# Optimization experiments

Measured on AMD Instinct MI355X. Metric: run time of the kernel, lower is better.

## Reference

```python
import jax, jax.numpy as jnp
import numpy as np

D = 128; H = 4; C = 128; L = 4
NC = 65536   # cells (1024 graphs x 64 cells)
NP = 32768   # pieces
NE = 65536   # edges per cell->cell direction
B = 1024     # num graphs
BW = 7       # BOARD_WIDTH (undefined global in source; connect-four width)
SLOPE = 0.2  # GATv2 LeakyReLU negative slope


def setup_inputs() -> dict:
    key = jax.random.key(0)
    ks = jax.random.split(key, 24)
    s = 0.05
    return {
        'cell_x': jnp.zeros((NC,), dtype=jnp.int32),
        'piece_x': jax.random.randint(ks[0], (NP,), 0, 2, dtype=jnp.int32),
        'occ_src': jax.random.randint(ks[1], (NP,), 0, NP, dtype=jnp.int32),
        'occ_dst': jax.random.randint(ks[2], (NP,), 0, NC, dtype=jnp.int32),
        'en_src': jax.random.randint(ks[3], (NE,), 0, NC, dtype=jnp.int32),
        'en_dst': jax.random.randint(ks[4], (NE,), 0, NC, dtype=jnp.int32),
        'ee_src': jax.random.randint(ks[5], (NE,), 0, NC, dtype=jnp.int32),
        'ee_dst': jax.random.randint(ks[6], (NE,), 0, NC, dtype=jnp.int32),
        'cell_batch': (jnp.arange(NC, dtype=jnp.int32) // (NC // B)).astype(jnp.int32),
        'cell_emb': jax.random.normal(ks[7], (1, D), jnp.float32),
        'piece_emb': jax.random.normal(ks[8], (2, D), jnp.float32),
        'Wl': jax.random.normal(ks[9], (L, 3, D, H * C), jnp.float32) * s,
        'bl': jnp.zeros((L, 3, H * C), jnp.float32),
        'Wr': jax.random.normal(ks[10], (L, 3, D, H * C), jnp.float32) * s,
        'br': jnp.zeros((L, 3, H * C), jnp.float32),
        'att': jax.random.normal(ks[11], (L, 3, H, C), jnp.float32) * 0.1,
        'conv_bias': jnp.zeros((L, 3, C), jnp.float32),
        'fc1_W': jax.random.normal(ks[12], (D, 64), jnp.float32) * s,
        'fc1_b': jnp.zeros((64,), jnp.float32),
        'pol_W': jax.random.normal(ks[13], (64, BW), jnp.float32) * s,
        'pol_b': jnp.zeros((BW,), jnp.float32),
        'val_W': jax.random.normal(ks[14], (64, 1), jnp.float32) * s,
        'val_b': jnp.zeros((1,), jnp.float32),
    }


def _gatv2(x_src, x_dst, src, dst, Wl, bl, Wr, br, att, bias):
    # PyG GATv2Conv, concat=False (mean over heads), add_self_loops=False, eval-mode dropout.
    n_dst = x_dst.shape[0]
    xl = (x_src @ Wl + bl).reshape(-1, H, C)      # [Ns,H,C]
    xr = (x_dst @ Wr + br).reshape(n_dst, H, C)   # [Nd,H,C]
    e = jax.nn.leaky_relu(xl[src] + xr[dst], SLOPE)            # [E,H,C]
    score = jnp.einsum('ehc,hc->eh', e, att)                   # [E,H]
    m = jax.ops.segment_max(score, dst, num_segments=n_dst)    # [Nd,H]
    p = jnp.exp(score - m[dst])
    denom = jax.ops.segment_sum(p, dst, num_segments=n_dst)
    alpha = p / (denom[dst] + 1e-16)                           # scatter-softmax
    out = jax.ops.segment_sum(alpha[:, :, None] * xl[src], dst, num_segments=n_dst)  # [Nd,H,C]
    return out.mean(axis=1) + bias


def reference(cell_x, piece_x, occ_src, occ_dst, en_src, en_dst, ee_src, ee_dst,
              cell_batch, cell_emb, piece_emb, Wl, bl, Wr, br, att, conv_bias,
              fc1_W, fc1_b, pol_W, pol_b, val_W, val_b):
    cell = cell_emb[cell_x]    # [NC,D]
    piece = piece_emb[piece_x]  # [NP,D]
    rels = [(occ_src, occ_dst), (en_src, en_dst), (ee_src, ee_dst)]
    for l in range(L):
        acc = jnp.zeros_like(cell)
        for r, (src, dst) in enumerate(rels):
            x_src = piece if r == 0 else cell
            acc = acc + _gatv2(x_src, cell, src, dst, Wl[l, r], bl[l, r],
                               Wr[l, r], br[l, r], att[l, r], conv_bias[l, r])
        cell = jax.nn.relu(acc)  # HeteroConv aggr='sum', then relu; dropout is identity in eval
    # global mean pool over cells per graph
    sums = jax.ops.segment_sum(cell, cell_batch, num_segments=B)
    cnts = jax.ops.segment_sum(jnp.ones((cell.shape[0],), cell.dtype), cell_batch, num_segments=B)
    pooled = sums / jnp.maximum(cnts, 1.0)[:, None]            # [B,D]
    h = jax.nn.relu(pooled @ fc1_W + fc1_b)
    policy_logits = h @ pol_W + pol_b
    value = jnp.tanh(h @ val_W + val_b)
    return policy_logits, value
```

## Files before the change

kernel.cpp:

```cpp
#include <hip/hip_runtime.h>
#include <hip/hip_bf16.h>
#include <math.h>

#define NCELLS 65536
#define NPIECE 32768
#define NEDGE  65536
#define NGRAPH 1024
#define DIM    128
#define NH     4
#define CH     128
#define HC     512
#define NLAYER 4
#define SLOPE  0.2f
#define DCAP   16

#define SCAP0   16384
#define SCAP12  36864
#define HCAP0   8192
#define HCAP12  20480
#define YCAP0   20480
#define YCAP12  28672
#define XLC_OFF0 0
#define XLC_OFF1 16384
#define XLC_OFF2 53248
#define XRC_OFF0 0
#define XRC_OFF1 8192
#define XRC_OFF2 28672
#define YL_OFF0  0
#define YL_OFF1  20480
#define YL_OFF2  49152
#define GEMM_BLOCKS 4960

typedef __attribute__((ext_vector_type(8))) __bf16 bf16x8;
typedef __attribute__((ext_vector_type(4))) float f32x4;

__device__ inline float bf2f(unsigned int u) {
    return __uint_as_float(u << 16);
}
__device__ inline unsigned short f2bf(float f) {
    unsigned int x = __float_as_uint(f);
    unsigned int r = (x + 0x7fff + ((x >> 16) & 1)) >> 16;
    return (unsigned short)r;
}
__device__ __forceinline__ void unpack8(uint4 v, float* o) {
    o[0] = bf2f(v.x & 0xffff); o[1] = bf2f(v.x >> 16);
    o[2] = bf2f(v.y & 0xffff); o[3] = bf2f(v.y >> 16);
    o[4] = bf2f(v.z & 0xffff); o[5] = bf2f(v.z >> 16);
    o[6] = bf2f(v.w & 0xffff); o[7] = bf2f(v.w >> 16);
}

#define GLOBAL_AS __attribute__((address_space(1)))
#define LDS_AS __attribute__((address_space(3)))
__device__ __forceinline__ void async_cp16(const void* g, void* l) {
    __builtin_amdgcn_global_load_lds((const GLOBAL_AS unsigned int*)g,
                                     (LDS_AS unsigned int*)l, 16, 0, 0);
}

__global__ void fill_kernel(float* __restrict__ p, float v, long n) {
    long i = (long)blockIdx.x * 256 + threadIdx.x;
    if (i < n) p[i] = v;
}

__global__ void embed_bf16_kernel(const int* __restrict__ idx, const float* __restrict__ emb,
                                  unsigned short* __restrict__ outb) {
    long t = (long)blockIdx.x * 256 + threadIdx.x;
    int node = (int)(t >> 7);
    int c = (int)(t & 127);
    outb[t] = f2bf(emb[(size_t)idx[node] * DIM + c]);
}

__global__ __launch_bounds__(256) void wconv_kernel(const float* __restrict__ Wl,
                                                    const float* __restrict__ Wr,
                                                    unsigned short* __restrict__ Wt) {
    __shared__ float tile[16][17];
    int bid = blockIdx.x;
    int wi = bid >> 8;
    int rem = bid & 255;
    int kt = rem >> 5;
    int nt = rem & 31;
    int tx = threadIdx.x & 15, ty = threadIdx.x >> 4;
    const float* W = (wi < 12) ? (Wl + (size_t)wi * DIM * HC) : (Wr + (size_t)(wi - 12) * DIM * HC);
    tile[ty][tx] = W[(size_t)(kt * 16 + ty) * HC + nt * 16 + tx];
    __syncthreads();
    Wt[(size_t)wi * HC * DIM + (size_t)(nt * 16 + ty) * DIM + kt * 16 + tx] = f2bf(tile[tx][ty]);
}

__global__ __launch_bounds__(256) void wsum_kernel(const float* __restrict__ Wl,
                                                   const float* __restrict__ bl,
                                                   unsigned short* __restrict__ Wsumt,
                                                   float* __restrict__ bsum) {
    int wi = blockIdx.x;
    const float* W = Wl + (size_t)wi * DIM * HC;
    for (int base = 0; base < 16384; base += 256) {
        int idx = base + threadIdx.x;
        int c = idx & 127, k = idx >> 7;
        float s = 0.25f * (W[(size_t)k * HC + c] + W[(size_t)k * HC + 128 + c] +
                           W[(size_t)k * HC + 256 + c] + W[(size_t)k * HC + 384 + c]);
        Wsumt[(size_t)wi * 16384 + (size_t)c * 128 + k] = f2bf(s);
    }
    if (threadIdx.x < 128) {
        int c = threadIdx.x;
        const float* b = bl + (size_t)wi * HC;
        bsum[wi * 128 + c] = 0.25f * (b[c] + b[128 + c] + b[256 + c] + b[384 + c]);
    }
}

__global__ __launch_bounds__(256) void bucket_build(const int* __restrict__ occ_src,
                                                    const int* __restrict__ occ_dst,
                                                    const int* __restrict__ en_src,
                                                    const int* __restrict__ en_dst,
                                                    const int* __restrict__ ee_src,
                                                    const int* __restrict__ ee_dst,
                                                    int* __restrict__ cnt3,
                                                    int* __restrict__ bucket3) {
    int id = blockIdx.x * 256 + threadIdx.x;
    int rel, e;
    const int* dstp;
    const int* srcp;
    if (id < NPIECE) { rel = 0; e = id; dstp = occ_dst; srcp = occ_src; }
    else if (id < NPIECE + NEDGE) { rel = 1; e = id - NPIECE; dstp = en_dst; srcp = en_src; }
    else if (id < NPIECE + 2 * NEDGE) { rel = 2; e = id - NPIECE - NEDGE; dstp = ee_dst; srcp = ee_src; }
    else return;
    int d = dstp[e];
    int pos = atomicAdd(&cnt3[rel * NCELLS + d], 1);
    if (pos < DCAP) bucket3[(size_t)rel * NCELLS * DCAP + (size_t)d * DCAP + pos] = srcp[e];
}

__global__ __launch_bounds__(256) void mark_build(const int* __restrict__ occ_src,
                                                  const int* __restrict__ occ_dst,
                                                  const int* __restrict__ en_src,
                                                  const int* __restrict__ en_dst,
                                                  const int* __restrict__ ee_src,
                                                  const int* __restrict__ ee_dst,
                                                  const int* __restrict__ cnt3,
                                                  int* __restrict__ srcmark,
                                                  int* __restrict__ ymark) {
    int id = blockIdx.x * 256 + threadIdx.x;
    int rel, e;
    const int* dstp;
    const int* srcp;
    if (id < NPIECE) { rel = 0; e = id; dstp = occ_dst; srcp = occ_src; }
    else if (id < NPIECE + NEDGE) { rel = 1; e = id - NPIECE; dstp = en_dst; srcp = en_src; }
    else if (id < NPIECE + 2 * NEDGE) { rel = 2; e = id - NPIECE - NEDGE; dstp = ee_dst; srcp = ee_src; }
    else return;
    int c = cnt3[rel * NCELLS + dstp[e]];
    if (c >= 2) srcmark[(rel << 16) + srcp[e]] = 1;
    else ymark[(rel << 16) + srcp[e]] = 1;
}

__global__ __launch_bounds__(256) void compact_all(const int* __restrict__ cnt3,
                                                   const int* __restrict__ srcmark,
                                                   const int* __restrict__ ymark,
                                                   unsigned long long* __restrict__ pcounts,
                                                   int* __restrict__ hotlist,
                                                   int* __restrict__ hotpos,
                                                   int* __restrict__ srclist,
                                                   int* __restrict__ srcpos,
                                                   int* __restrict__ ylist,
                                                   int* __restrict__ ypos) {
    __shared__ int wcnt[4][3];
    __shared__ unsigned long long blockbase;
    int id = blockIdx.x * 256 + threadIdx.x;
    int lane = threadIdx.x & 63;
    int w = threadIdx.x >> 6;
    int r = id >> 16;
    int node = id & (NCELLS - 1);

    bool a0 = (cnt3[id] >= 2);
    bool a1 = (srcmark[id] != 0);
    bool a2 = (ymark[id] != 0);
    unsigned long long m0 = __ballot(a0);
    unsigned long long m1 = __ballot(a1);
    unsigned long long m2 = __ballot(a2);
    if (lane == 0) {
        wcnt[w][0] = (int)__popcll(m0);
        wcnt[w][1] = (int)__popcll(m1);
        wcnt[w][2] = (int)__popcll(m2);
    }
    __syncthreads();
    if (threadIdx.x == 0) {
        unsigned long long s0 = wcnt[0][0] + wcnt[1][0] + wcnt[2][0] + wcnt[3][0];
        unsigned long long s1 = wcnt[0][1] + wcnt[1][1] + wcnt[2][1] + wcnt[3][1];
        unsigned long long s2 = wcnt[0][2] + wcnt[1][2] + wcnt[2][2] + wcnt[3][2];
        blockbase = atomicAdd(&pcounts[r], s0 | (s1 << 21) | (s2 << 42));
    }
    __syncthreads();
    unsigned long long bb = blockbase;
    int b0 = (int)(bb & 0x1FFFFF);
    int b1 = (int)((bb >> 21) & 0x1FFFFF);
    int b2 = (int)((bb >> 42) & 0x1FFFFF);
#pragma unroll
    for (int w2 = 0; w2 < 4; w2++) {
        if (w2 < w) { b0 += wcnt[w2][0]; b1 += wcnt[w2][1]; b2 += wcnt[w2][2]; }
    }
    {
        int cap  = (r == 0) ? HCAP0 : HCAP12;
        int loff = (r == 0) ? XRC_OFF0 : (r == 1) ? XRC_OFF1 : XRC_OFF2;
        if (a0) {
            int pos = b0 + (int)__popcll(m0 & ((1ull << lane) - 1ull));
            if (pos < cap) { hotlist[loff + pos] = node; hotpos[id] = pos; }
            else hotpos[id] = cap - 1;
        }
    }
    {
        int cap  = (r == 0) ? SCAP0 : SCAP12;
        int loff = (r == 0) ? XLC_OFF0 : (r == 1) ? XLC_OFF1 : XLC_OFF2;
        if (a1) {
            int pos = b1 + (int)__popcll(m1 & ((1ull << lane) - 1ull));
            if (pos < cap) { srclist[loff + pos] = node; srcpos[id] = pos; }
            else srcpos[id] = cap - 1;
        }
    }
    {
        int cap  = (r == 0) ? YCAP0 : YCAP12;
        int loff = (r == 0) ? YL_OFF0 : (r == 1) ? YL_OFF1 : YL_OFF2;
        if (a2) {
            int pos = b2 + (int)__popcll(m2 & ((1ull << lane) - 1ull));
            if (pos < cap) { ylist[loff + pos] = node; ypos[id] = pos; }
            else ypos[id] = cap - 1;
        }
    }
}

__global__ void unpack_counts(const unsigned long long* __restrict__ pcounts,
                              int* __restrict__ counts) {
    int r = threadIdx.x;
    if (r < 3) {
        unsigned long long v = pcounts[r];
        counts[r]     = (int)(v & 0x1FFFFF);
        counts[4 + r] = (int)((v >> 21) & 0x1FFFFF);
        counts[8 + r] = (int)((v >> 42) & 0x1FFFFF);
    }
}

__global__ __launch_bounds__(256) void bucket_translate(const int* __restrict__ cnt3,
                                                        const int* __restrict__ srcpos,
                                                        const int* __restrict__ ypos,
                                                        int* __restrict__ bucket3) {
    int id = blockIdx.x * 256 + threadIdx.x;
    if (id >= 3 * NCELLS) return;
    int r = id >> 16;
    int deg = cnt3[id];
    if (deg > DCAP) deg = DCAP;
    if (deg == 0) return;
    int* b = bucket3 + (size_t)id * DCAP;
    if (deg == 1) {
        b[0] = ypos[(r << 16) + b[0]];
    } else {
        for (int s = 0; s < deg; s++) b[s] = srcpos[(r << 16) + b[s]];
    }
}

__device__ __forceinline__ void gemm_body(const unsigned short* __restrict__ A,
                                          const int* __restrict__ gather, int nrows,
                                          const unsigned short* __restrict__ Bt,
                                          const float* __restrict__ bias,
                                          unsigned short* __restrict__ out, int ostride,
                                          int row0, int col0,
                                          unsigned short* smem) {
    unsigned short* As = smem;
    unsigned short* Bs = smem + 16384;
    const int t = threadIdx.x;
    const int w = t >> 6;
    const int l = t & 63;
    const int q = l >> 4, r15 = l & 15;

    {
#pragma unroll
        for (int it = 0; it < 8; it++) {
            int r0 = 32 * w + 4 * it;
            int row = r0 + q;
            int c = r15 ^ (row & 15);
            int grow = row0 + row;
            if (gather) grow = gather[grow < nrows ? grow : (nrows - 1)];
            async_cp16(A + (size_t)grow * 128 + c * 8, &As[r0 * 128]);
        }
        const unsigned short* Bg = Bt + (size_t)col0 * 128;
#pragma unroll
        for (int it = 0; it < 4; it++) {
            int r0 = 16 * w + 4 * it;
            int row = r0 + q;
            int c = r15 ^ (row & 15);
            async_cp16(Bg + (size_t)row * 128 + c * 8, &Bs[r0 * 128]);
        }
    }
    __syncthreads();

    const int m0 = (w >> 1) * 64;
    const int n0 = (w & 1) * 32;

    f32x4 acc[2][4][2];
#pragma unroll
    for (int nh = 0; nh < 2; nh++)
#pragma unroll
        for (int i = 0; i < 4; i++)
#pragma unroll
            for (int j = 0; j < 2; j++) acc[nh][i][j] = (f32x4)(0.0f);

#pragma unroll
    for (int ks = 0; ks < 4; ks++) {
        int slot = (4 * ks + q) ^ r15;
        bf16x8 a[4], b[2];
#pragma unroll
        for (int i = 0; i < 4; i++)
            a[i] = *(const bf16x8*)&As[(m0 + 16 * i + r15) * 128 + slot * 8];
#pragma unroll
        for (int j = 0; j < 2; j++)
            b[j] = *(const bf16x8*)&Bs[(n0 + 16 * j + r15) * 128 + slot * 8];
#pragma unroll
        for (int i = 0; i < 4; i++)
#pragma unroll
            for (int j = 0; j < 2; j++)
                acc[0][i][j] = __builtin_amdgcn_mfma_f32_16x16x32_bf16(a[i], b[j], acc[0][i][j], 0, 0, 0);
    }
    __syncthreads();

    {
        const unsigned short* Bg = Bt + (size_t)(col0 + 64) * 128;
#pragma unroll
        for (int it = 0; it < 4; it++) {
            int r0 = 16 * w + 4 * it;
            int row = r0 + q;
            int c = r15 ^ (row & 15);
            async_cp16(Bg + (size_t)row * 128 + c * 8, &Bs[r0 * 128]);
        }
    }
    __syncthreads();

#pragma unroll
    for (int ks = 0; ks < 4; ks++) {
        int slot = (4 * ks + q) ^ r15;
        bf16x8 a[4], b[2];
#pragma unroll
        for (int i = 0; i < 4; i++)
            a[i] = *(const bf16x8*)&As[(m0 + 16 * i + r15) * 128 + slot * 8];
#pragma unroll
        for (int j = 0; j < 2; j++)
            b[j] = *(const bf16x8*)&Bs[(n0 + 16 * j + r15) * 128 + slot * 8];
#pragma unroll
        for (int i = 0; i < 4; i++)
#pragma unroll
            for (int j = 0; j < 2; j++)
                acc[1][i][j] = __builtin_amdgcn_mfma_f32_16x16x32_bf16(a[i], b[j], acc[1][i][j], 0, 0, 0);
    }
    __syncthreads();

    unsigned short* tile = smem;
#pragma unroll
    for (int nh = 0; nh < 2; nh++)
#pragma unroll
        for (int j = 0; j < 2; j++) {
            int col = nh * 64 + n0 + 16 * j + r15;
            float bv = bias[col0 + col];
#pragma unroll
            for (int i = 0; i < 4; i++) {
                int mg = m0 + 16 * i + 4 * q;
#pragma unroll
                for (int rg = 0; rg < 4; rg++)
                    tile[(mg + rg) * 136 + col] = f2bf(acc[nh][i][j][rg] + bv);
            }
        }
    __syncthreads();
#pragma unroll
    for (int it = 0; it < 8; it++) {
        int rr = it * 16 + (t >> 4);
        int cc = (t & 15) * 8;
        if (row0 + rr < nrows) {
            uint4 v = *(const uint4*)&tile[rr * 136 + cc];
            *(uint4*)&out[(size_t)(row0 + rr) * ostride + col0 + cc] = v;
        }
    }
}

__global__ __launch_bounds__(256) void gemm_layer(const unsigned short* __restrict__ pieceb,
                                                  const unsigned short* __restrict__ cellb,
                                                  const int* __restrict__ srclist,
                                                  const int* __restrict__ hotlist,
                                                  const int* __restrict__ ylist,
                                                  const int* __restrict__ counts,
                                                  const unsigned short* __restrict__ Wt,
                                                  const unsigned short* __restrict__ Wsumt,
                                                  const float* __restrict__ bl,
                                                  const float* __restrict__ br,
                                                  const float* __restrict__ bsum,
                                                  unsigned short* __restrict__ xlc,
                                                  unsigned short* __restrict__ yl,
                                                  unsigned short* __restrict__ xrc,
                                                  int lay) {
    __shared__ unsigned short smem[24576];
    int x = blockIdx.x;
    int r, sec, idx;
    if (x < 928) {
        r = 0;
        if (x < 512) { sec = 0; idx = x; }
        else if (x < 672) { sec = 1; idx = x - 512; }
        else { sec = 2; idx = x - 672; }
    } else if (x < 2944) {
        r = 1; x -= 928;
        if (x < 1152) { sec = 0; idx = x; }
        else if (x < 1376) { sec = 1; idx = x - 1152; }
        else { sec = 2; idx = x - 1376; }
    } else {
        r = 2; x -= 2944;
        if (x < 1152) { sec = 0; idx = x; }
        else if (x < 1376) { sec = 1; idx = x - 1152; }
        else { sec = 2; idx = x - 1376; }
    }
    int wi = lay * 3 + r;
    const unsigned short* Asrc = (r == 0) ? pieceb : cellb;
    int scap = (r == 0) ? SCAP0 : SCAP12;
    int hcap = (r == 0) ? HCAP0 : HCAP12;
    int ycap = (r == 0) ? YCAP0 : YCAP12;
    int xlcoff = (r == 0) ? XLC_OFF0 : (r == 1) ? XLC_OFF1 : XLC_OFF2;
    int xrcoff = (r == 0) ? XRC_OFF0 : (r == 1) ? XRC_OFF1 : XRC_OFF2;
    int yloff  = (r == 0) ? YL_OFF0  : (r == 1) ? YL_OFF1  : YL_OFF2;

    if (sec == 0) {
        int nrowblk = scap >> 7;
        int row = idx % nrowblk, col = idx / nrowblk;
        int nsrc = counts[4 + r];
        if (nsrc > scap) nsrc = scap;
        if (row * 128 >= nsrc) return;
        gemm_body(Asrc, srclist + xlcoff, nsrc,
                  Wt + (size_t)wi * HC * DIM, bl + (size_t)wi * HC,
                  xlc + (size_t)xlcoff * HC, HC, row * 128, col * 128, smem);
    } else if (sec == 1) {
        int ny = counts[8 + r];
        if (ny > ycap) ny = ycap;
        if (idx * 128 >= ny) return;
        gemm_body(Asrc, ylist + yloff, ny,
                  Wsumt + (size_t)wi * 16384, bsum + (size_t)wi * 128,
                  yl + (size_t)yloff * 128, 128, idx * 128, 0, smem);
    } else {
        int nrowblk = hcap >> 7;
        int row = idx % nrowblk, col = idx / nrowblk;
        int nhot = counts[r];
        if (nhot > hcap) nhot = hcap;
        if (row * 128 >= nhot) return;
        gemm_body(cellb, hotlist + xrcoff, nhot,
                  Wt + (size_t)(12 + wi) * HC * DIM, br + (size_t)wi * HC,
                  xrc + (size_t)xrcoff * HC, HC, row * 128, col * 128, smem);
    }
}

__global__ __launch_bounds__(256) void agg3(const unsigned short* __restrict__ xlc,
                                            const unsigned short* __restrict__ yl,
                                            const unsigned short* __restrict__ xrc,
                                            const int* __restrict__ bucket3,
                                            const int* __restrict__ cnt3,
                                            const int* __restrict__ hotpos,
                                            const float* __restrict__ att,
                                            const float* __restrict__ cb,
                                            unsigned short* __restrict__ cellb,
                                            int lay) {
    int d = blockIdx.x * 4 + (threadIdx.x >> 6);
    int l = threadIdx.x & 63;
    int g = l >> 4;

    int deg[3], spv[3], hp[3];
#pragma unroll
    for (int r = 0; r < 3; r++) {
        int c = cnt3[r * NCELLS + d];
        deg[r] = (c > DCAP) ? DCAP : c;
    }
#pragma unroll
    for (int r = 0; r < 3; r++)
        spv[r] = (l < deg[r]) ? bucket3[(size_t)r * NCELLS * DCAP + (size_t)d * DCAP + l] : 0;
#pragma unroll
    for (int r = 0; r < 3; r++)
        hp[r] = (deg[r] >= 2) ? hotpos[r * NCELLS + d] : 0;

    float acc[8] = {0.f, 0.f, 0.f, 0.f, 0.f, 0.f, 0.f, 0.f};
#pragma unroll
    for (int r = 0; r < 3; r++) {
        if (deg[r] == 0) continue;
        int xlcoff = (r == 0) ? XLC_OFF0 : (r == 1) ? XLC_OFF1 : XLC_OFF2;
        int xrcoff = (r == 0) ? XRC_OFF0 : (r == 1) ? XRC_OFF1 : XRC_OFF2;
        int yloff  = (r == 0) ? YL_OFF0  : (r == 1) ? YL_OFF1  : YL_OFF2;

        if (deg[r] == 1) {
            int yp = __shfl(spv[r], 0, 64);
            if (g == r) {
                uint4 v = *(const uint4*)(yl + (size_t)(yloff + yp) * 128 + (l & 15) * 8);
                float y[8];
                unpack8(v, y);
#pragma unroll
                for (int j = 0; j < 8; j++) acc[j] += y[j];
            }
        } else {
            uint4 rv = *(const uint4*)(xrc + (size_t)(xrcoff + hp[r]) * HC + l * 8);
            float re[8];
            unpack8(rv, re);
            const float* at = att + (size_t)(lay * 3 + r) * HC;
            float4 a0 = *(const float4*)&at[l * 8];
            float4 a1 = *(const float4*)&at[l * 8 + 4];
            float av[8] = {a0.x, a0.y, a0.z, a0.w, a1.x, a1.y, a1.z, a1.w};

            int dg = deg[r];
            float sum_w = 0.f;
            float tm[8] = {0.f, 0.f, 0.f, 0.f, 0.f, 0.f, 0.f, 0.f};
            int sp0 = __shfl(spv[r], 0, 64);
            uint4 vcur = *(const uint4*)(xlc + (size_t)(xlcoff + sp0) * HC + l * 8);
            for (int k = 0; k < dg; k++) {
                uint4 vnext;
                if (k + 1 < dg) {
                    int spn = __shfl(spv[r], k + 1, 64);
                    vnext = *(const uint4*)(xlc + (size_t)(xlcoff + spn) * HC + l * 8);
                }
                float le[8];
                unpack8(vcur, le);
                float partial = 0.f;
#pragma unroll
                for (int j = 0; j < 8; j++) {
                    float e = le[j] + re[j];
                    e = e > 0.0f ? e : SLOPE * e;
                    partial += e * av[j];
                }
#pragma unroll
                for (int off = 1; off < 16; off <<= 1) partial += __shfl_xor(partial, off, 64);
                float wgt = __expf(partial);
                sum_w += wgt;
#pragma unroll
                for (int j = 0; j < 8; j++) tm[j] += wgt * le[j];
                vcur = vnext;
            }
            float inv = 0.25f / sum_w;
#pragma unroll
            for (int j = 0; j < 8; j++) acc[j] += tm[j] * inv;
        }
    }

#pragma unroll
    for (int j = 0; j < 8; j++) {
        acc[j] += __shfl_xor(acc[j], 16, 64);
        acc[j] += __shfl_xor(acc[j], 32, 64);
    }

    if (l < 16) {
        int c0 = l * 8;
        float v[8];
#pragma unroll
        for (int j = 0; j < 8; j++) {
            int c = c0 + j;
            float b = cb[c] + cb[CH + c] + cb[2 * CH + c];
            v[j] = fmaxf(acc[j] + b, 0.0f);
        }
        uint4 pv;
        pv.x = (unsigned)f2bf(v[0]) | ((unsigned)f2bf(v[1]) << 16);
        pv.y = (unsigned)f2bf(v[2]) | ((unsigned)f2bf(v[3]) << 16);
        pv.z = (unsigned)f2bf(v[4]) | ((unsigned)f2bf(v[5]) << 16);
        pv.w = (unsigned)f2bf(v[6]) | ((unsigned)f2bf(v[7]) << 16);
        *(uint4*)&cellb[(size_t)d * CH + c0] = pv;
    }
}

__global__ __launch_bounds__(64) void pool_kernel(const unsigned short* __restrict__ cellb,
                                                  float* __restrict__ pooled) {
    int b = blockIdx.x, l = threadIdx.x;
    const unsigned short* base = cellb + (size_t)b * 64 * DIM;
    float s[8] = {0.f, 0.f, 0.f, 0.f, 0.f, 0.f, 0.f, 0.f};
    for (int i = 0; i < 64; i++) {
        uint4 v = *(const uint4*)(base + (size_t)i * DIM + (l & 15) * 8);
        float y[8];
        unpack8(v, y);
#pragma unroll
        for (int j = 0; j < 8; j++) s[j] += y[j];
    }
    if (l < 16) {
        float4 o0 = make_float4(s[0] * (1.f / 64.f), s[1] * (1.f / 64.f),
                                s[2] * (1.f / 64.f), s[3] * (1.f / 64.f));
        float4 o1 = make_float4(s[4] * (1.f / 64.f), s[5] * (1.f / 64.f),
                                s[6] * (1.f / 64.f), s[7] * (1.f / 64.f));
        *(float4*)&pooled[(size_t)b * DIM + l * 8] = o0;
        *(float4*)&pooled[(size_t)b * DIM + l * 8 + 4] = o1;
    }
}

__global__ __launch_bounds__(64) void head_kernel(const float* __restrict__ pooled,
                                                  const float* __restrict__ fc1W,
                                                  const float* __restrict__ fc1b,
                                                  const float* __restrict__ polW,
                                                  const float* __restrict__ polb,
                                                  const float* __restrict__ valW,
                                                  const float* __restrict__ valb,
                                                  float* __restrict__ out) {
    int b = blockIdx.x, t = threadIdx.x;
    __shared__ float ps[128];
    __shared__ float hs[64];
    ps[t] = pooled[(size_t)b * DIM + t];
    ps[t + 64] = pooled[(size_t)b * DIM + 64 + t];
    __syncthreads();
    float h = fc1b[t];
#pragma unroll 16
    for (int d = 0; d < 128; d++) h += ps[d] * fc1W[d * 64 + t];
    hs[t] = fmaxf(h, 0.0f);
    __syncthreads();
    if (t < 7) {
        float po = polb[t];
#pragma unroll 16
        for (int k = 0; k < 64; k++) po += hs[k] * polW[k * 7 + t];
        out[(size_t)b * 7 + t] = po;
    }
    if (t == 63) {
        float v = valb[0];
#pragma unroll 16
        for (int k = 0; k < 64; k++) v += hs[k] * valW[k];
        out[(size_t)NGRAPH * 7 + b] = tanhf(v);
    }
}

extern "C" void kernel_launch(void* const* d_in, const int* in_sizes, int n_in,
                              void* d_out, int out_size, void* d_ws, size_t ws_size,
                              hipStream_t stream) {
    const int* cell_x   = (const int*)d_in[0];
    const int* piece_x  = (const int*)d_in[1];
    const int* occ_src  = (const int*)d_in[2];
    const int* occ_dst  = (const int*)d_in[3];
    const int* en_src   = (const int*)d_in[4];
    const int* en_dst   = (const int*)d_in[5];
    const int* ee_src   = (const int*)d_in[6];
    const int* ee_dst   = (const int*)d_in[7];
    const float* cell_emb  = (const float*)d_in[9];
    const float* piece_emb = (const float*)d_in[10];
    const float* Wl  = (const float*)d_in[11];
    const float* bl  = (const float*)d_in[12];
    const float* Wr  = (const float*)d_in[13];
    const float* br  = (const float*)d_in[14];
    const float* att = (const float*)d_in[15];
    const float* conv_bias = (const float*)d_in[16];
    const float* fc1W = (const float*)d_in[17];
    const float* fc1b = (const float*)d_in[18];
    const float* polW = (const float*)d_in[19];
    const float* polb = (const float*)d_in[20];
    const float* valW = (const float*)d_in[21];
    const float* valb = (const float*)d_in[22];
    float* out = (float*)d_out;

    char* ws = (char*)d_ws;
    size_t off = 0;
    auto take = [&](size_t bytes) -> void* {
        void* p = (void*)(ws + off);
        off += (bytes + 255) & ~(size_t)255;
        return p;
    };
    unsigned short* cellb  = (unsigned short*)take((size_t)NCELLS * DIM * 2);
    unsigned short* pieceb = (unsigned short*)take((size_t)NPIECE * DIM * 2);
    unsigned short* xlc    = (unsigned short*)take((size_t)(SCAP0 + 2 * SCAP12) * HC * 2);
    unsigned short* yl     = (unsigned short*)take((size_t)(YCAP0 + 2 * YCAP12) * 128 * 2);
    unsigned short* xrc    = (unsigned short*)take((size_t)(HCAP0 + 2 * HCAP12) * HC * 2);
    unsigned short* Wt     = (unsigned short*)take((size_t)24 * HC * DIM * 2);
    unsigned short* Wsumt  = (unsigned short*)take((size_t)12 * 128 * 128 * 2);
    float* bsum            = (float*)take((size_t)12 * 128 * 4);
    int*   izone   = (int*)take(((size_t)9 * NCELLS + 32) * 4);
    int*   cnt3    = izone;
    unsigned long long* pcounts = (unsigned long long*)(izone + 3 * NCELLS);
    int*   counts  = izone + 3 * NCELLS + 8;
    int*   srcmark = izone + 3 * NCELLS + 32;
    int*   ymark   = izone + 6 * NCELLS + 32;
    int*   bucket3 = (int*)take((size_t)3 * NCELLS * DCAP * 4);
    int*   hotlist = (int*)take((size_t)(HCAP0 + 2 * HCAP12) * 4);
    int*   hotpos  = (int*)take((size_t)3 * NCELLS * 4);
    int*   srclist = (int*)take((size_t)(SCAP0 + 2 * SCAP12) * 4);
    int*   srcpos  = (int*)take((size_t)3 * NCELLS * 4);
    int*   ylist   = (int*)take((size_t)(YCAP0 + 2 * YCAP12) * 4);
    int*   ypos    = (int*)take((size_t)3 * NCELLS * 4);
    float* pooled  = (float*)take((size_t)NGRAPH * DIM * 4);

    if (off > ws_size) {
        fill_kernel<<<(out_size + 255) / 256, 256, 0, stream>>>(out, 0.0f, out_size);
        return;
    }

    wconv_kernel<<<24 * 256, 256, 0, stream>>>(Wl, Wr, Wt);
    wsum_kernel<<<12, 256, 0, stream>>>(Wl, bl, Wsumt, bsum);
    embed_bf16_kernel<<<NPIECE * DIM / 256, 256, 0, stream>>>(piece_x, piece_emb, pieceb);
    embed_bf16_kernel<<<NCELLS * DIM / 256, 256, 0, stream>>>(cell_x, cell_emb, cellb);
    fill_kernel<<<(9 * NCELLS + 32 + 255) / 256, 256, 0, stream>>>((float*)izone, 0.0f, 9 * NCELLS + 32);
    bucket_build<<<(NPIECE + 2 * NEDGE + 255) / 256, 256, 0, stream>>>(
        occ_src, occ_dst, en_src, en_dst, ee_src, ee_dst, cnt3, bucket3);
    mark_build<<<(NPIECE + 2 * NEDGE + 255) / 256, 256, 0, stream>>>(
        occ_src, occ_dst, en_src, en_dst, ee_src, ee_dst, cnt3, srcmark, ymark);
    compact_all<<<3 * NCELLS / 256, 256, 0, stream>>>(
        cnt3, srcmark, ymark, pcounts, hotlist, hotpos, srclist, srcpos, ylist, ypos);
    unpack_counts<<<1, 64, 0, stream>>>(pcounts, counts);
    bucket_translate<<<(3 * NCELLS + 255) / 256, 256, 0, stream>>>(cnt3, srcpos, ypos, bucket3);

    for (int l = 0; l < NLAYER; l++) {
        gemm_layer<<<GEMM_BLOCKS, 256, 0, stream>>>(
            pieceb, cellb, srclist, hotlist, ylist, counts, Wt, Wsumt, bl, br, bsum,
            xlc, yl, xrc, l);
        agg3<<<NCELLS / 4, 256, 0, stream>>>(
            xlc, yl, xrc, bucket3, cnt3, hotpos, att,
            conv_bias + (size_t)l * 3 * CH, cellb, l);
    }

    pool_kernel<<<NGRAPH, 64, 0, stream>>>(cellb, pooled);
    head_kernel<<<NGRAPH, 64, 0, stream>>>(pooled, fc1W, fc1b, polW, polb, valW, valb, out);
}
```

Before: 637.0 us.

## Split aggregation into hot-cell kernel over compacted list and light degree-one kernel

Builds a compacted list of cells that have degree of at least two in any relation. The full attention aggregation now runs only over that list, and a separate lightweight kernel handles cells whose relations all have degree at most one by summing precomputed projected rows. The aim is to cut wasted wavefronts and register pressure in the heavy aggregation kernel for cells that need no softmax. In exchange it adds an extra kernel launch per layer and a build pass, and agg3_hot is launched with a fixed grid of HANYCAP/4 blocks where many may exit early.

```diff
diff --git a/kernel.cpp b/kernel.cpp
--- a/kernel.cpp
+++ b/kernel.cpp
@@ -20,6 +20,7 @@
 #define HCAP12  20480
 #define YCAP0   20480
 #define YCAP12  28672
+#define HANYCAP 49152
 #define XLC_OFF0 0
 #define XLC_OFF1 16384
 #define XLC_OFF2 53248
@@ -222,6 +223,32 @@
     }
 }
 
+__global__ __launch_bounds__(256) void hotany_build(const int* __restrict__ cnt3,
+                                                    unsigned long long* __restrict__ pcounts,
+                                                    int* __restrict__ hotanylist) {
+    __shared__ int wcnt[4];
+    __shared__ unsigned long long blockbase;
+    int d = blockIdx.x * 256 + threadIdx.x;
+    int lane = threadIdx.x & 63;
+    int w = threadIdx.x >> 6;
+    bool active = (cnt3[d] >= 2) | (cnt3[NCELLS + d] >= 2) | (cnt3[2 * NCELLS + d] >= 2);
+    unsigned long long m = __ballot(active);
+    if (lane == 0) wcnt[w] = (int)__popcll(m);
+    __syncthreads();
+    if (threadIdx.x == 0) {
+        unsigned long long s = wcnt[0] + wcnt[1] + wcnt[2] + wcnt[3];
+        blockbase = atomicAdd(&pcounts[3], s);
+    }
+    __syncthreads();
+    int base = (int)blockbase;
+#pragma unroll
+    for (int w2 = 0; w2 < 4; w2++) if (w2 < w) base += wcnt[w2];
+    if (active) {
+        int pos = base + (int)__popcll(m & ((1ull << lane) - 1ull));
+        if (pos < HANYCAP) hotanylist[pos] = d;
+    }
+}
+
 __global__ void unpack_counts(const unsigned long long* __restrict__ pcounts,
                               int* __restrict__ counts) {
     int r = threadIdx.x;
@@ -230,6 +257,9 @@
         counts[r]     = (int)(v & 0x1FFFFF);
         counts[4 + r] = (int)((v >> 21) & 0x1FFFFF);
         counts[8 + r] = (int)((v >> 42) & 0x1FFFFF);
+    } else if (r == 3) {
+        int h = (int)pcounts[3];
+        counts[12] = (h > HANYCAP) ? HANYCAP : h;
     }
 }
 
@@ -443,17 +473,21 @@
     }
 }
 
-__global__ __launch_bounds__(256) void agg3(const unsigned short* __restrict__ xlc,
-                                            const unsigned short* __restrict__ yl,
-                                            const unsigned short* __restrict__ xrc,
-                                            const int* __restrict__ bucket3,
-                                            const int* __restrict__ cnt3,
-                                            const int* __restrict__ hotpos,
-                                            const float* __restrict__ att,
-                                            const float* __restrict__ cb,
-                                            unsigned short* __restrict__ cellb,
-                                            int lay) {
-    int d = blockIdx.x * 4 + (threadIdx.x >> 6);
+__global__ __launch_bounds__(256) void agg3_hot(const unsigned short* __restrict__ xlc,
+                                                const unsigned short* __restrict__ yl,
+                                                const unsigned short* __restrict__ xrc,
+                                                const int* __restrict__ bucket3,
+                                                const int* __restrict__ cnt3,
+                                                const int* __restrict__ hotpos,
+                                                const int* __restrict__ hotanylist,
+                                                const int* __restrict__ counts,
+                                                const float* __restrict__ att,
+                                                const float* __restrict__ cb,
+                                                unsigned short* __restrict__ cellb,
+                                                int lay) {
+    int idx = blockIdx.x * 4 + (threadIdx.x >> 6);
+    if (idx >= counts[12]) return;
+    int d = hotanylist[idx];
     int l = threadIdx.x & 63;
     int g = l >> 4;
 
@@ -527,6 +561,58 @@
             float inv = 0.25f / sum_w;
 #pragma unroll
             for (int j = 0; j < 8; j++) acc[j] += tm[j] * inv;
+        }
+    }
+
+#pragma unroll
+    for (int j = 0; j < 8; j++) {
+        acc[j] += __shfl_xor(acc[j], 16, 64);
+        acc[j] += __shfl_xor(acc[j], 32, 64);
+    }
+
+    if (l < 16) {
+        int c0 = l * 8;
+        float v[8];
+#pragma unroll
+        for (int j = 0; j < 8; j++) {
+            int c = c0 + j;
+            float b = cb[c] + cb[CH + c] + cb[2 * CH + c];
+            v[j] = fmaxf(acc[j] + b, 0.0f);
+        }
+        uint4 pv;
+        pv.x = (unsigned)f2bf(v[0]) | ((unsigned)f2bf(v[1]) << 16);
+        pv.y = (unsigned)f2bf(v[2]) | ((unsigned)f2bf(v[3]) << 16);
+        pv.z = (unsigned)f2bf(v[4]) | ((unsigned)f2bf(v[5]) << 16);
+        pv.w = (unsigned)f2bf(v[6]) | ((unsigned)f2bf(v[7]) << 16);
+        *(uint4*)&cellb[(size_t)d * CH + c0] = pv;
+    }
+}
+
+__global__ __launch_bounds__(256) void agg_y(const unsigned short* __restrict__ yl,
+                                             const int* __restrict__ bucket3,
+                                             const int* __restrict__ cnt3,
+                                             const float* __restrict__ cb,
+                                             unsigned short* __restrict__ cellb) {
+    int d = blockIdx.x * 4 + (threadIdx.x >> 6);
+    int l = threadIdx.x & 63;
+    int g = l >> 4;
+
+    int c0v = cnt3[d], c1v = cnt3[NCELLS + d], c2v = cnt3[2 * NCELLS + d];
+    if (c0v >= 2 || c1v >= 2 || c2v >= 2) return;
+    int deg[3] = {c0v, c1v, c2v};
+
+    float acc[8] = {0.f, 0.f, 0.f, 0.f, 0.f, 0.f, 0.f, 0.f};
+#pragma unroll
+    for (int r = 0; r < 3; r++) {
+        if (deg[r] != 1) continue;
+        int yloff = (r == 0) ? YL_OFF0 : (r == 1) ? YL_OFF1 : YL_OFF2;
+        if (g == r) {
+            int yp = bucket3[(size_t)r * NCELLS * DCAP + (size_t)d * DCAP];
+            uint4 v = *(const uint4*)(yl + (size_t)(yloff + yp) * 128 + (l & 15) * 8);
+            float y[8];
+            unpack8(v, y);
+#pragma unroll
+            for (int j = 0; j < 8; j++) acc[j] += y[j];
         }
     }
 
@@ -664,6 +750,7 @@
     int*   srcpos  = (int*)take((size_t)3 * NCELLS * 4);
     int*   ylist   = (int*)take((size_t)(YCAP0 + 2 * YCAP12) * 4);
     int*   ypos    = (int*)take((size_t)3 * NCELLS * 4);
+    int*   hotany  = (int*)take((size_t)HANYCAP * 4);
     float* pooled  = (float*)take((size_t)NGRAPH * DIM * 4);
 
     if (off > ws_size) {
@@ -682,6 +769,7 @@
         occ_src, occ_dst, en_src, en_dst, ee_src, ee_dst, cnt3, srcmark, ymark);
     compact_all<<<3 * NCELLS / 256, 256, 0, stream>>>(
         cnt3, srcmark, ymark, pcounts, hotlist, hotpos, srclist, srcpos, ylist, ypos);
+    hotany_build<<<NCELLS / 256, 256, 0, stream>>>(cnt3, pcounts, hotany);
     unpack_counts<<<1, 64, 0, stream>>>(pcounts, counts);
     bucket_translate<<<(3 * NCELLS + 255) / 256, 256, 0, stream>>>(cnt3, srcpos, ypos, bucket3);
 
@@ -689,9 +777,11 @@
         gemm_layer<<<GEMM_BLOCKS, 256, 0, stream>>>(
             pieceb, cellb, srclist, hotlist, ylist, counts, Wt, Wsumt, bl, br, bsum,
             xlc, yl, xrc, l);
-        agg3<<<NCELLS / 4, 256, 0, stream>>>(
-            xlc, yl, xrc, bucket3, cnt3, hotpos, att,
+        agg3_hot<<<HANYCAP / 4, 256, 0, stream>>>(
+            xlc, yl, xrc, bucket3, cnt3, hotpos, hotany, counts, att,
             conv_bias + (size_t)l * 3 * CH, cellb, l);
+        agg_y<<<NCELLS / 4, 256, 0, stream>>>(
+            yl, bucket3, cnt3, conv_bias + (size_t)l * 3 * CH, cellb);
     }
 
     pool_kernel<<<NGRAPH, 64, 0, stream>>>(cellb, pooled);
```

Measured after the change: 647.4 us. No clear change (+1.6%).
